# Performance work log

Measured on AMD Instinct MI355X. Metric: run time of the kernel, lower is better.

The kernel has to match this reference:

```python
import jax, jax.numpy as jnp
import numpy as np

FEAT_DIM = 1024
NUM_HEAD = 8


def setup_inputs() -> dict:
    key = jax.random.key(0)
    ks = jax.random.split(key, 8)
    D = FEAT_DIM
    s = D ** -0.5
    return {
        "motion": jax.random.normal(ks[0], (8, 1024, D), dtype=jnp.float32),
        "scene_feats": jax.random.normal(ks[1], (8, 2048, D), dtype=jnp.float32),
        # nn.Linear weights stored as [in, out] (already transposed for x @ W)
        "Wq": jax.random.normal(ks[2], (D, D), dtype=jnp.float32) * s,
        "bq": jax.random.normal(ks[3], (D,), dtype=jnp.float32) * s,
        "Wkv": jax.random.normal(ks[4], (D, 2 * D), dtype=jnp.float32) * s,
        "bkv": jax.random.normal(ks[5], (2 * D,), dtype=jnp.float32) * s,
        "Wout": jax.random.normal(ks[6], (D, D), dtype=jnp.float32) * s,
        "bout": jax.random.normal(ks[7], (D,), dtype=jnp.float32) * s,
    }


def reference(motion, scene_feats, Wq, bq, Wkv, bkv, Wout, bout):
    bs, L, D = motion.shape
    N = scene_feats.shape[1]
    H = NUM_HEAD
    Dh = D // H

    # q scaled by full feat_dim**-0.5 (as in source, not head_dim)
    q = (motion @ Wq + bq) * (D ** -0.5)
    kv = scene_feats @ Wkv + bkv
    k, v = kv[..., :D], kv[..., D:]

    # Faithful to source: q is viewed as (bs, H, L, Dh) with NO transpose,
    # while k, v use view(bs, N, H, Dh) followed by transpose(1, 2).
    q = q.reshape(bs, H, L, Dh)                      # [bs,H,L,Dh] (layout quirk)
    k = k.reshape(bs, N, H, Dh).transpose(0, 2, 1, 3)  # [bs,H,N,Dh]
    v = v.reshape(bs, N, H, Dh).transpose(0, 2, 1, 3)  # [bs,H,N,Dh]

    att = jnp.einsum("bhld,bhnd->bhln", q, k)        # [bs,H,L,N]
    att = jax.nn.softmax(att, axis=-1)
    out = jnp.einsum("bhln,bhnd->bhld", att, v)      # [bs,H,L,Dh]
    out = out.reshape(bs, L, D)                      # contiguous view, matches torch .view
    return out @ Wout + bout
```

## Files before the change

kernel.cpp:

```cpp
#include <hip/hip_runtime.h>

typedef __attribute__((ext_vector_type(8))) short bf16x8;
typedef __attribute__((ext_vector_type(4))) float f32x4;
typedef __attribute__((ext_vector_type(4))) float f32x4v;

#define MFMA16(a,b,c) __builtin_amdgcn_mfma_f32_16x16x32_bf16((a),(b),(c),0,0,0)

__device__ __forceinline__ short f2bf(float f){
  unsigned u = __builtin_bit_cast(unsigned, f);
  u += 0x7fffu + ((u >> 16) & 1u);
  return (short)(u >> 16);
}

__device__ __forceinline__ void gload16(const void* g, void* l){
  __builtin_amdgcn_global_load_lds((const __attribute__((address_space(1))) unsigned*)g,
                                   (__attribute__((address_space(3))) unsigned*)l,
                                   16, 0, 0);
}

__global__ __launch_bounds__(256) void k_f2bf(const float* __restrict__ in,
                                              short* __restrict__ out, int n8){
  int i = blockIdx.x * 256 + threadIdx.x;
  if (i >= n8) return;
  f32x4v a = ((const f32x4v*)in)[i*2];
  f32x4v b = ((const f32x4v*)in)[i*2+1];
  bf16x8 o;
  o[0]=f2bf(a[0]); o[1]=f2bf(a[1]); o[2]=f2bf(a[2]); o[3]=f2bf(a[3]);
  o[4]=f2bf(b[0]); o[5]=f2bf(b[1]); o[6]=f2bf(b[2]); o[7]=f2bf(b[3]);
  ((bf16x8*)out)[i] = o;
}

__global__ __launch_bounds__(256) void k_prep_wT(const float* __restrict__ W,
                                                 short* __restrict__ Wt, int K, int N){
  int i = blockIdx.x * 256 + threadIdx.x;
  int total = (K >> 3) * N;
  if (i >= total) return;
  int n  = i % N;
  int k0 = (i / N) << 3;
  bf16x8 o;
#pragma unroll
  for (int j = 0; j < 8; ++j) o[j] = f2bf(W[(size_t)(k0 + j) * N + n]);
  *(bf16x8*)&Wt[(size_t)n * K + k0] = o;
}

template<int MODE>
__global__ __launch_bounds__(256, 2) void k_gemm(
    const short* __restrict__ A, const short* __restrict__ Bt,
    const float* __restrict__ bias, float scale,
    void* __restrict__ out0, void* __restrict__ out1,
    int M, int N, int K)
{
  __shared__ __align__(16) short Alds[2][128 * 32];
  __shared__ __align__(16) short Blds[2][128 * 32];
  const int tid = threadIdx.x;
  const int l = tid & 63, w = tid >> 6;
  const int m0 = blockIdx.y * 128, n0 = blockIdx.x * 128;
  const int wr = w >> 1, wc = w & 1;
  const int lr = l & 15, lg = l >> 4;

  const int srow = l >> 2;
  const int scol = 8 * ((l & 3) ^ (srow & 3));
  const int acol = 8 * (lg ^ (lr & 3));

  f32x4 acc[4][4];
#pragma unroll
  for (int a = 0; a < 4; ++a)
#pragma unroll
    for (int b = 0; b < 4; ++b) acc[a][b] = (f32x4)(0.0f);

  const int nk = K >> 5;
  auto stage = [&](int kt, int buf){
    int k0 = kt << 5;
#pragma unroll
    for (int i = 0; i < 4; ++i){
      int c = w * 4 + i;
      if (c < 8){
        int m = c * 16 + srow;
        gload16(A + (size_t)(m0 + m) * K + k0 + scol, &Alds[buf][c * 512]);
      } else {
        int n = (c - 8) * 16 + srow;
        gload16(Bt + (size_t)(n0 + n) * K + k0 + scol, &Blds[buf][(c - 8) * 512]);
      }
    }
  };

  stage(0, 0);
  __syncthreads();
  int cur = 0;
  for (int kt = 0; kt < nk; ++kt){
    if (kt + 1 < nk) stage(kt + 1, cur ^ 1);
    bf16x8 af[4], bfv[4];
#pragma unroll
    for (int mi = 0; mi < 4; ++mi){
      int row = wr * 64 + mi * 16 + lr;
      af[mi] = *(const bf16x8*)&Alds[cur][row * 32 + acol];
    }
#pragma unroll
    for (int ni = 0; ni < 4; ++ni){
      int row = wc * 64 + ni * 16 + lr;
      bfv[ni] = *(const bf16x8*)&Blds[cur][row * 32 + acol];
    }
#pragma unroll
    for (int mi = 0; mi < 4; ++mi)
#pragma unroll
      for (int ni = 0; ni < 4; ++ni)
        acc[mi][ni] = MFMA16(af[mi], bfv[ni], acc[mi][ni]);
    __syncthreads();
    cur ^= 1;
  }

#pragma unroll
  for (int mi = 0; mi < 4; ++mi)
#pragma unroll
    for (int ni = 0; ni < 4; ++ni){
      int col = n0 + wc * 64 + ni * 16 + lr;
      float bv = bias[col];
#pragma unroll
      for (int r = 0; r < 4; ++r){
        int row = m0 + wr * 64 + mi * 16 + lg * 4 + r;
        float v = acc[mi][ni][r] + bv;
        if (MODE == 0){
          v *= scale;
          int b = row >> 10, lp = row & 1023;
          int h = lp >> 7;
          int lq = ((lp & 127) << 3) | (col >> 7);
          int dh = col & 127;
          ((short*)out0)[(((size_t)(b * 8 + h)) * 1024 + lq) * 128 + dh] = f2bf(v);
        } else if (MODE == 1){
          int b = row >> 11, nn = row & 2047;
          if (col < 1024){
            int h = col >> 7, dh = col & 127;
            ((short*)out0)[(((size_t)(b * 8 + h)) * 2048 + nn) * 128 + dh] = f2bf(v);
          } else {
            int c2 = col - 1024, h = c2 >> 7, dh = c2 & 127;
            ((short*)out1)[(((size_t)(b * 8 + h)) * 128 + dh) * 2048 + nn] = f2bf(v);
          }
        } else {
          ((float*)out0)[(size_t)row * N + col] = v;
        }
      }
    }
}

__global__ __launch_bounds__(256, 2) void k_attn(
    const short* __restrict__ Q, const short* __restrict__ K,
    const short* __restrict__ Vt, short* __restrict__ O)
{
  __shared__ __align__(16) short Klds[2][64 * 128];
  __shared__ __align__(16) short Vlds[2][128 * 64];
  __shared__ __align__(16) short Plds[4][32 * 64];
  const int tid = threadIdx.x;
  const int l = tid & 63, w = tid >> 6;
  const int lr = l & 15, lg = l >> 4;

  int flat = blockIdx.y * 8 + blockIdx.x;
  int xcd = flat & 7, idx = flat >> 3;
  int bh = xcd * 8 + (idx >> 3);
  int q0 = (idx & 7) * 128;

  const short* Qb = Q  + (size_t)bh * 1024 * 128;
  const short* Kb = K  + (size_t)bh * 2048 * 128;
  const short* Vb = Vt + (size_t)bh * 128 * 2048;

  bf16x8 qf[2][4];
#pragma unroll
  for (int mi = 0; mi < 2; ++mi)
#pragma unroll
    for (int kc = 0; kc < 4; ++kc)
      qf[mi][kc] = *(const bf16x8*)&Qb[(size_t)(q0 + w * 32 + mi * 16 + lr) * 128 + kc * 32 + lg * 8];

  f32x4 acc[8][2];
#pragma unroll
  for (int d = 0; d < 8; ++d){ acc[d][0] = (f32x4)(0.0f); acc[d][1] = (f32x4)(0.0f); }
  float mrun[2][4], lsum[2][4];
#pragma unroll
  for (int mi = 0; mi < 2; ++mi)
#pragma unroll
    for (int r = 0; r < 4; ++r){ mrun[mi][r] = -3e38f; lsum[mi][r] = 0.f; }

  auto stageK = [&](int t, int buf){
    int kv0 = t * 64;
#pragma unroll
    for (int i = 0; i < 4; ++i){
      int c = w * 4 + i;
      int row = 4 * c + (l >> 4);
      int col = ((l & 15) * 8) ^ ((row & 7) * 8);
      gload16(Kb + (size_t)(kv0 + row) * 128 + col, &Klds[buf][c * 512]);
    }
  };
  auto stageV = [&](int t, int buf){
    int kv0 = t * 64;
#pragma unroll
    for (int i = 0; i < 4; ++i){
      int c = w * 4 + i;
      int dh = 8 * c + (l >> 3);
      int col = ((l & 7) * 8) ^ (((l >> 3) & 7) * 8);
      gload16(Vb + (size_t)dh * 2048 + kv0 + col, &Vlds[buf][c * 512]);
    }
  };

  stageK(0, 0); stageV(0, 0);
  __syncthreads();
  int cur = 0;
  const int swz = (lr & 7) * 8;

  for (int t = 0; t < 32; ++t){
    if (t + 1 < 32){ stageK(t + 1, cur ^ 1); stageV(t + 1, cur ^ 1); }
    const short* Kl = &Klds[cur][0];
    const short* Vl = &Vlds[cur][0];
    short* Pw = &Plds[w][0];

    f32x4 s[2][4];
#pragma unroll
    for (int nt = 0; nt < 4; ++nt){
      f32x4 s0 = (f32x4)(0.0f), s1 = (f32x4)(0.0f);
#pragma unroll
      for (int kc = 0; kc < 4; ++kc){
        bf16x8 kf = *(const bf16x8*)&Kl[(nt * 16 + lr) * 128 + ((kc * 32 + lg * 8) ^ swz)];
        s0 = MFMA16(qf[0][kc], kf, s0);
        s1 = MFMA16(qf[1][kc], kf, s1);
      }
      s[0][nt] = s0; s[1][nt] = s1;
    }

    float pmax[2][4];
    int ok = 1;
#pragma unroll
    for (int mi = 0; mi < 2; ++mi)
#pragma unroll
      for (int r = 0; r < 4; ++r){
        float v = fmaxf(fmaxf(s[mi][0][r], s[mi][1][r]), fmaxf(s[mi][2][r], s[mi][3][r]));
        pmax[mi][r] = v;
        ok &= (v <= mrun[mi][r] + 8.0f) ? 1 : 0;
      }
    if (!__all(ok)){
#pragma unroll
      for (int mi = 0; mi < 2; ++mi)
#pragma unroll
        for (int r = 0; r < 4; ++r){
          float v = pmax[mi][r];
          v = fmaxf(v, __shfl_xor(v, 1, 16));
          v = fmaxf(v, __shfl_xor(v, 2, 16));
          v = fmaxf(v, __shfl_xor(v, 4, 16));
          v = fmaxf(v, __shfl_xor(v, 8, 16));
          float mnew = fmaxf(mrun[mi][r], v);
          float sc = exp2f(mrun[mi][r] - mnew);
          mrun[mi][r] = mnew;
          lsum[mi][r] *= sc;
#pragma unroll
          for (int d = 0; d < 8; ++d) acc[d][mi][r] *= sc;
        }
    }

#pragma unroll
    for (int mi = 0; mi < 2; ++mi)
#pragma unroll
      for (int r = 0; r < 4; ++r){
        int row = mi * 16 + lg * 4 + r;
        int rsw = (row & 7) * 8;
        float ls = 0.f;
#pragma unroll
        for (int nt = 0; nt < 4; ++nt){
          float p = exp2f(s[mi][nt][r] - mrun[mi][r]);
          ls += p;
          Pw[row * 64 + ((nt * 16 + lr) ^ rsw)] = f2bf(p);
        }
        lsum[mi][r] += ls;
      }

    bf16x8 pa[2][2];
#pragma unroll
    for (int mi = 0; mi < 2; ++mi)
#pragma unroll
      for (int kc = 0; kc < 2; ++kc)
        pa[mi][kc] = *(const bf16x8*)&Pw[(mi * 16 + lr) * 64 + ((kc * 32 + lg * 8) ^ swz)];
#pragma unroll
    for (int d = 0; d < 8; ++d)
#pragma unroll
      for (int kc = 0; kc < 2; ++kc){
        bf16x8 vf = *(const bf16x8*)&Vl[(d * 16 + lr) * 64 + ((kc * 32 + lg * 8) ^ swz)];
        acc[d][0] = MFMA16(pa[0][kc], vf, acc[d][0]);
        acc[d][1] = MFMA16(pa[1][kc], vf, acc[d][1]);
      }

    __syncthreads();
    cur ^= 1;
  }

  const int b = bh >> 3, h = bh & 7;
#pragma unroll
  for (int mi = 0; mi < 2; ++mi)
#pragma unroll
    for (int r = 0; r < 4; ++r){
      float ls = lsum[mi][r];
      ls += __shfl_xor(ls, 1, 16);
      ls += __shfl_xor(ls, 2, 16);
      ls += __shfl_xor(ls, 4, 16);
      ls += __shfl_xor(ls, 8, 16);
      float inv = 1.0f / ls;
      int grow = q0 + w * 32 + mi * 16 + lg * 4 + r;
      size_t base = ((size_t)b * 1024 + (size_t)h * 128 + (grow >> 3)) * 1024
                  + (size_t)(grow & 7) * 128;
#pragma unroll
      for (int d = 0; d < 8; ++d)
        O[base + d * 16 + lr] = f2bf(acc[d][mi][r] * inv);
    }
}

extern "C" void kernel_launch(void* const* d_in, const int* in_sizes, int n_in,
                              void* d_out, int out_size, void* d_ws, size_t ws_size,
                              hipStream_t stream){
  const float* motion = (const float*)d_in[0];
  const float* scene  = (const float*)d_in[1];
  const float* Wq     = (const float*)d_in[2];
  const float* bq     = (const float*)d_in[3];
  const float* Wkv    = (const float*)d_in[4];
  const float* bkv    = (const float*)d_in[5];
  const float* Wout   = (const float*)d_in[6];
  const float* bout   = (const float*)d_in[7];
  float* out = (float*)d_out;

  char* ws = (char*)d_ws;
  const size_t MB = 1024 * 1024;
  short* WqT   = (short*)(ws + 0);
  short* WkvT  = (short*)(ws + 2  * MB);
  short* WoutT = (short*)(ws + 6  * MB);
  short* mA    = (short*)(ws + 8  * MB);
  short* sA    = (short*)(ws + 24 * MB);
  short* Qb    = (short*)(ws + 56 * MB);
  short* Kb    = (short*)(ws + 72 * MB);
  short* Vtb   = (short*)(ws + 104* MB);
  short* attnO = mA;

  const float qscale = 0.03125f * 1.44269504088896341f;

  k_prep_wT<<<dim3(512),  256, 0, stream>>>(Wq,   WqT,   1024, 1024);
  k_prep_wT<<<dim3(1024), 256, 0, stream>>>(Wkv,  WkvT,  1024, 2048);
  k_prep_wT<<<dim3(512),  256, 0, stream>>>(Wout, WoutT, 1024, 1024);
  k_f2bf<<<dim3(4096), 256, 0, stream>>>(motion, mA, 1024 * 1024);
  k_f2bf<<<dim3(8192), 256, 0, stream>>>(scene,  sA, 2 * 1024 * 1024);

  k_gemm<0><<<dim3(8, 64),   256, 0, stream>>>(mA, WqT,  bq,  qscale, Qb, nullptr, 8192, 1024, 1024);
  k_gemm<1><<<dim3(16, 128), 256, 0, stream>>>(sA, WkvT, bkv, 1.0f,   Kb, Vtb,    16384, 2048, 1024);
  k_attn<<<dim3(8, 64), 256, 0, stream>>>(Qb, Kb, Vtb, attnO);
  k_gemm<2><<<dim3(8, 64), 256, 0, stream>>>(attnO, WoutT, bout, 1.0f, out, nullptr, 8192, 1024, 1024);
}
```

Measured before the change: 345.1 us.

## Replace GEMM with 256x256-tile, 8-wave, phase-pipelined kernel with XCD remap

Replaces the 128x128 double-buffered GEMM with a 512-thread 256x256 tile kernel. It splits each 64-wide K step into two 32-wide halves, interleaves LDS fragment loads, async global-to-LDS staging and MFMA phases under explicit barriers and s_waitcnt, and raises wave priority around the MFMA blocks. It also remaps workgroup IDs across the XCDs for cache locality and adds setprio around the attention MFMA loops. The larger tile cuts global traffic per FLOP, at the cost of a hard-coded K=1024, more LDS (64 KB) and fewer workgroups, which may lower occupancy on the smaller GEMMs.

New measurement: 350.3 us. About the same (+1.5%).

```diff
diff --git a/kernel.cpp b/kernel.cpp
--- a/kernel.cpp
+++ b/kernel.cpp
@@ -44,102 +44,143 @@
 }
 
 template<int MODE>
-__global__ __launch_bounds__(256, 2) void k_gemm(
+__global__ __launch_bounds__(512, 2) void k_gemm256(
     const short* __restrict__ A, const short* __restrict__ Bt,
     const float* __restrict__ bias, float scale,
-    void* __restrict__ out0, void* __restrict__ out1,
-    int M, int N, int K)
+    void* __restrict__ out0, void* __restrict__ out1, int Ncols)
 {
-  __shared__ __align__(16) short Alds[2][128 * 32];
-  __shared__ __align__(16) short Blds[2][128 * 32];
+  __shared__ __align__(16) short As[2][2][256 * 32];
+  __shared__ __align__(16) short Bs[2][2][256 * 32];
   const int tid = threadIdx.x;
   const int l = tid & 63, w = tid >> 6;
-  const int m0 = blockIdx.y * 128, n0 = blockIdx.x * 128;
-  const int wr = w >> 1, wc = w & 1;
   const int lr = l & 15, lg = l >> 4;
-
-  const int srow = l >> 2;
-  const int scol = 8 * ((l & 3) ^ (srow & 3));
-  const int acol = 8 * (lg ^ (lr & 3));
-
-  f32x4 acc[4][4];
-#pragma unroll
-  for (int a = 0; a < 4; ++a)
+  const int wm = w >> 2, wn = w & 3;
+
+  const int nx = gridDim.x;
+  const int nwg = nx * gridDim.y;
+  int flat = blockIdx.y * nx + blockIdx.x;
+  int u = (flat & 7) * (nwg >> 3) + (flat >> 3);
+  const int m0 = (u / nx) * 256, n0 = (u % nx) * 256;
+
+  int srow[2], scol[2];
+#pragma unroll
+  for (int i = 0; i < 2; ++i){
+    int p = (w * 2 + i) * 64 + l;
+    int row = p >> 2, g = p & 3;
+    srow[i] = row;
+    scol[i] = (g ^ ((row >> 1) & 3)) * 8;
+  }
+  auto stageA = [&](int tt, int kk, int slot){
+#pragma unroll
+    for (int i = 0; i < 2; ++i)
+      gload16(A + (size_t)(m0 + srow[i]) * 1024 + tt * 64 + kk * 32 + scol[i],
+              &As[slot][kk][(w * 2 + i) * 512]);
+  };
+  auto stageB = [&](int tt, int kk, int slot){
+#pragma unroll
+    for (int i = 0; i < 2; ++i)
+      gload16(Bt + (size_t)(n0 + srow[i]) * 1024 + tt * 64 + kk * 32 + scol[i],
+              &Bs[slot][kk][(w * 2 + i) * 512]);
+  };
+
+  f32x4 acc[8][4];
+#pragma unroll
+  for (int a = 0; a < 8; ++a)
 #pragma unroll
     for (int b = 0; b < 4; ++b) acc[a][b] = (f32x4)(0.0f);
 
-  const int nk = K >> 5;
-  auto stage = [&](int kt, int buf){
-    int k0 = kt << 5;
-#pragma unroll
-    for (int i = 0; i < 4; ++i){
-      int c = w * 4 + i;
-      if (c < 8){
-        int m = c * 16 + srow;
-        gload16(A + (size_t)(m0 + m) * K + k0 + scol, &Alds[buf][c * 512]);
-      } else {
-        int n = (c - 8) * 16 + srow;
-        gload16(Bt + (size_t)(n0 + n) * K + k0 + scol, &Blds[buf][(c - 8) * 512]);
-      }
-    }
-  };
-
-  stage(0, 0);
-  __syncthreads();
-  int cur = 0;
-  for (int kt = 0; kt < nk; ++kt){
-    if (kt + 1 < nk) stage(kt + 1, cur ^ 1);
-    bf16x8 af[4], bfv[4];
-#pragma unroll
-    for (int mi = 0; mi < 4; ++mi){
-      int row = wr * 64 + mi * 16 + lr;
-      af[mi] = *(const bf16x8*)&Alds[cur][row * 32 + acol];
-    }
+  bf16x8 af[4], bfr[4];
+#define LOADA(bb, kk, mh)                                                       \
+  {_Pragma("unroll")                                                            \
+   for (int mi = 0; mi < 4; ++mi){                                              \
+     int row = wm * 128 + (mh) * 64 + mi * 16 + lr;                             \
+     af[mi] = *(const bf16x8*)&As[bb][kk][row * 32 + ((lg ^ ((row >> 1) & 3)) * 8)]; }}
+#define LOADB(bb, kk)                                                           \
+  {_Pragma("unroll")                                                            \
+   for (int ni = 0; ni < 4; ++ni){                                              \
+     int row = wn * 64 + ni * 16 + lr;                                          \
+     bfr[ni] = *(const bf16x8*)&Bs[bb][kk][row * 32 + ((lg ^ ((row >> 1) & 3)) * 8)]; }}
+#define MFMA_PHASE(mh)                                                          \
+  {_Pragma("unroll")                                                            \
+   for (int mi = 0; mi < 4; ++mi)                                               \
+     _Pragma("unroll")                                                          \
+     for (int ni = 0; ni < 4; ++ni)                                             \
+       acc[(mh) * 4 + mi][ni] = MFMA16(af[mi], bfr[ni], acc[(mh) * 4 + mi][ni]);}
+#define SBAR() { __builtin_amdgcn_sched_barrier(0); __builtin_amdgcn_s_barrier(); \
+                 __builtin_amdgcn_sched_barrier(0); }
+
+  const int nt = 16;
+  stageA(0, 0, 0); stageB(0, 0, 0);
+  stageA(0, 1, 0); stageB(0, 1, 0);
+  stageA(1, 0, 1); stageB(1, 0, 1);
+  asm volatile("s_waitcnt vmcnt(8)");
+  SBAR();
+
+  for (int t = 0; t < nt; ++t){
+    const int b = t & 1;
+    const int t1 = (t + 1 < nt) ? t + 1 : nt - 1;
+    const int t2 = (t + 2 < nt) ? t + 2 : nt - 1;
+    LOADB(b, 0); LOADA(b, 0, 0);
+    stageA(t1, 1, b ^ 1);
+    SBAR();
+    __builtin_amdgcn_s_setprio(1); MFMA_PHASE(0); __builtin_amdgcn_s_setprio(0);
+    SBAR();
+    LOADA(b, 0, 1);
+    stageB(t1, 1, b ^ 1);
+    SBAR();
+    __builtin_amdgcn_s_setprio(1); MFMA_PHASE(1); __builtin_amdgcn_s_setprio(0);
+    __builtin_amdgcn_sched_barrier(0);
+    asm volatile("s_waitcnt vmcnt(8)");
+    SBAR();
+    LOADB(b, 1); LOADA(b, 1, 0);
+    stageA(t2, 0, b);
+    SBAR();
+    __builtin_amdgcn_s_setprio(1); MFMA_PHASE(0); __builtin_amdgcn_s_setprio(0);
+    SBAR();
+    LOADA(b, 1, 1);
+    stageB(t2, 0, b);
+    SBAR();
+    __builtin_amdgcn_s_setprio(1); MFMA_PHASE(1); __builtin_amdgcn_s_setprio(0);
+    __builtin_amdgcn_sched_barrier(0);
+    asm volatile("s_waitcnt vmcnt(8)");
+    SBAR();
+  }
+
+#pragma unroll
+  for (int mig = 0; mig < 8; ++mig)
 #pragma unroll
     for (int ni = 0; ni < 4; ++ni){
-      int row = wc * 64 + ni * 16 + lr;
-      bfv[ni] = *(const bf16x8*)&Blds[cur][row * 32 + acol];
-    }
-#pragma unroll
-    for (int mi = 0; mi < 4; ++mi)
-#pragma unroll
-      for (int ni = 0; ni < 4; ++ni)
-        acc[mi][ni] = MFMA16(af[mi], bfv[ni], acc[mi][ni]);
-    __syncthreads();
-    cur ^= 1;
-  }
-
-#pragma unroll
-  for (int mi = 0; mi < 4; ++mi)
-#pragma unroll
-    for (int ni = 0; ni < 4; ++ni){
-      int col = n0 + wc * 64 + ni * 16 + lr;
+      int col = n0 + wn * 64 + ni * 16 + lr;
       float bv = bias[col];
 #pragma unroll
       for (int r = 0; r < 4; ++r){
-        int row = m0 + wr * 64 + mi * 16 + lg * 4 + r;
-        float v = acc[mi][ni][r] + bv;
+        int row = m0 + wm * 128 + mig * 16 + lg * 4 + r;
+        float v = acc[mig][ni][r] + bv;
         if (MODE == 0){
           v *= scale;
-          int b = row >> 10, lp = row & 1023;
+          int bb = row >> 10, lp = row & 1023;
           int h = lp >> 7;
           int lq = ((lp & 127) << 3) | (col >> 7);
           int dh = col & 127;
-          ((short*)out0)[(((size_t)(b * 8 + h)) * 1024 + lq) * 128 + dh] = f2bf(v);
+          ((short*)out0)[(((size_t)(bb * 8 + h)) * 1024 + lq) * 128 + dh] = f2bf(v);
         } else if (MODE == 1){
-          int b = row >> 11, nn = row & 2047;
+          int bb = row >> 11, nn = row & 2047;
           if (col < 1024){
             int h = col >> 7, dh = col & 127;
-            ((short*)out0)[(((size_t)(b * 8 + h)) * 2048 + nn) * 128 + dh] = f2bf(v);
+            ((short*)out0)[(((size_t)(bb * 8 + h)) * 2048 + nn) * 128 + dh] = f2bf(v);
           } else {
             int c2 = col - 1024, h = c2 >> 7, dh = c2 & 127;
-            ((short*)out1)[(((size_t)(b * 8 + h)) * 128 + dh) * 2048 + nn] = f2bf(v);
+            ((short*)out1)[(((size_t)(bb * 8 + h)) * 128 + dh) * 2048 + nn] = f2bf(v);
           }
         } else {
-          ((float*)out0)[(size_t)row * N + col] = v;
+          ((float*)out0)[(size_t)row * Ncols + col] = v;
         }
       }
     }
+#undef LOADA
+#undef LOADB
+#undef MFMA_PHASE
+#undef SBAR
 }
 
 __global__ __launch_bounds__(256, 2) void k_attn(
@@ -211,6 +252,7 @@
     short* Pw = &Plds[w][0];
 
     f32x4 s[2][4];
+    __builtin_amdgcn_s_setprio(1);
 #pragma unroll
     for (int nt = 0; nt < 4; ++nt){
       f32x4 s0 = (f32x4)(0.0f), s1 = (f32x4)(0.0f);
@@ -222,6 +264,7 @@
       }
       s[0][nt] = s0; s[1][nt] = s1;
     }
+    __builtin_amdgcn_s_setprio(0);
 
     float pmax[2][4];
     int ok = 1;
@@ -274,6 +317,7 @@
 #pragma unroll
       for (int kc = 0; kc < 2; ++kc)
         pa[mi][kc] = *(const bf16x8*)&Pw[(mi * 16 + lr) * 64 + ((kc * 32 + lg * 8) ^ swz)];
+    __builtin_amdgcn_s_setprio(1);
 #pragma unroll
     for (int d = 0; d < 8; ++d)
 #pragma unroll
@@ -282,6 +326,7 @@
         acc[d][0] = MFMA16(pa[0][kc], vf, acc[d][0]);
         acc[d][1] = MFMA16(pa[1][kc], vf, acc[d][1]);
       }
+    __builtin_amdgcn_s_setprio(0);
 
     __syncthreads();
     cur ^= 1;
@@ -340,8 +385,8 @@
   k_f2bf<<<dim3(4096), 256, 0, stream>>>(motion, mA, 1024 * 1024);
   k_f2bf<<<dim3(8192), 256, 0, stream>>>(scene,  sA, 2 * 1024 * 1024);
 
-  k_gemm<0><<<dim3(8, 64),   256, 0, stream>>>(mA, WqT,  bq,  qscale, Qb, nullptr, 8192, 1024, 1024);
-  k_gemm<1><<<dim3(16, 128), 256, 0, stream>>>(sA, WkvT, bkv, 1.0f,   Kb, Vtb,    16384, 2048, 1024);
+  k_gemm256<0><<<dim3(4, 32), 512, 0, stream>>>(mA, WqT,  bq,  qscale, Qb, nullptr, 1024);
+  k_gemm256<1><<<dim3(8, 64), 512, 0, stream>>>(sA, WkvT, bkv, 1.0f,   Kb, Vtb,    2048);
   k_attn<<<dim3(8, 64), 256, 0, stream>>>(Qb, Kb, Vtb, attnO);
-  k_gemm<2><<<dim3(8, 64), 256, 0, stream>>>(attnO, WoutT, bout, 1.0f, out, nullptr, 8192, 1024, 1024);
-}
+  k_gemm256<2><<<dim3(4, 32), 512, 0, stream>>>(attnO, WoutT, bout, 1.0f, out, nullptr, 1024);
+}
```
